# Kernel tuning notes

Measured on AMD Instinct MI355X. Metric: run time of the kernel, lower is better.

The kernel has to match this reference:

```python
import jax, jax.numpy as jnp
import numpy as np

NUM_TABLES = 10  # distinct table_id values per item


def setup_inputs() -> dict:
    key = jax.random.key(0)
    ks = jax.random.split(key, 10)
    B, NL, P, TOK, D = 4, 2, 100, 60, 768
    T = P * TOK
    s = 0.02  # weight init scale
    return {
        "answer_states": jax.random.normal(ks[0], (B, NL, 1, D), jnp.float32),
        "query_passage_states": jax.random.normal(ks[1], (B, NL, T, D), jnp.float32),
        "passage_masks": jax.random.uniform(ks[2], (B, P, TOK), jnp.float32),
        "table_ids": jax.random.randint(ks[3], (B, P), 0, NUM_TABLES, jnp.int32),
        "Wp": jax.random.normal(ks[4], (D, 3 * D), jnp.float32) * s,
        "bp": jnp.zeros((D,), jnp.float32),
        "Wt": jax.random.normal(ks[5], (D, 3 * D), jnp.float32) * s,
        "bt": jnp.zeros((D,), jnp.float32),
        "Wf1": jax.random.normal(ks[6], (D, 2 * D), jnp.float32) * s,
        "bf1": jnp.zeros((D,), jnp.float32),
        "Wf2": jax.random.normal(ks[7], (1, D), jnp.float32) * s,
        "bf2": jnp.zeros((1,), jnp.float32),
    }


def reference(answer_states, query_passage_states, passage_masks, table_ids,
              Wp, bp, Wt, bt, Wf1, bf1, Wf2, bf2):
    # keep only the last layer, as in the torch code ([:, -1:, :, :])
    A = answer_states[:, -1:, :, :]                 # [B,1,1,D]
    Q = query_passage_states[:, -1:, :, :]          # [B,1,T,D]
    A = jnp.broadcast_to(A, Q.shape)                # expand over tokens
    x = jnp.concatenate([A, Q, A * Q], axis=-1)     # [B,1,T,3D]

    ps = jnp.einsum('bltk,dk->bltd', x, Wp) + bp    # passage_fnt  [B,1,T,D]
    ts = jnp.einsum('bltk,dk->bltd', x, Wt) + bt    # table_fnt    [B,1,T,D]

    B, L, T, D = ps.shape
    P, TOK = passage_masks.shape[1], passage_masks.shape[2]
    ps = ps.reshape(B, L, P, TOK, D)
    ts = ts.reshape(B, L, P, TOK, D)

    def table_aggr(states, ids):
        # states: [L,P,TOK,D]; segment-max over passages sharing a table_id,
        # then gather the aggregate back to every passage (the dict grouping).
        s = jnp.moveaxis(states, 1, 0)                       # [P,L,TOK,D]
        tmax = jnp.full((NUM_TABLES,) + s.shape[1:], -jnp.inf, s.dtype)
        tmax = tmax.at[ids].max(s)                           # [NT,L,TOK,D]
        return jnp.moveaxis(tmax[ids], 0, 1)                 # [L,P,TOK,D]

    aggr = jax.vmap(table_aggr)(ts, table_ids)               # [B,L,P,TOK,D]

    feat = jnp.concatenate([ps, aggr], axis=-1)              # [B,L,P,TOK,2D]
    h = jax.nn.relu(jnp.einsum('blptk,dk->blptd', feat, Wf1) + bf1)
    # dropout is identity in eval mode
    scores = (jnp.einsum('blptd,od->blpto', h, Wf2) + bf2)[..., 0]  # [B,L,P,TOK]

    masked = scores * passage_masks[:, None, :, :]           # mask expanded over layers
    return masked.sum(axis=(1, 3))                            # [B,P]
```

## Files before the change

### kernel.cpp

```cpp
#include <hip/hip_runtime.h>
#include <hip/hip_bf16.h>


typedef unsigned short u16;
typedef unsigned int u32;
typedef __attribute__((ext_vector_type(8))) short bf16x8;
typedef __attribute__((ext_vector_type(4))) float f32x4;

#define NUM_TABLES 10
#define MPAD 6016
#define DD 768

__device__ __forceinline__ u16 f2bf(float f) {
  u32 u = __builtin_bit_cast(u32, f);
  u32 r = u + 0x7FFFu + ((u >> 16) & 1u);
  return (u16)(r >> 16);
}
__device__ __forceinline__ float bf2f(u16 h) {
  u32 u = ((u32)h) << 16;
  return __builtin_bit_cast(float, u);
}
__device__ __forceinline__ u32 pack_bf2(float lo, float hi) {
  return (u32)f2bf(lo) | ((u32)f2bf(hi) << 16);
}

__device__ __forceinline__ void gload_lds16(const u16* g, u16* l) {
  __builtin_amdgcn_global_load_lds(
      (const __attribute__((address_space(1))) void*)g,
      (__attribute__((address_space(3))) void*)l, 16, 0, 0);
}

__global__ void prep_all(const float* __restrict__ qps, uint4* __restrict__ qpad,
                         const float* __restrict__ Ans, const float* __restrict__ Wp,
                         const float* __restrict__ Wt, u16* __restrict__ Wtb,
                         u16* __restrict__ WpbT,
                         const float* __restrict__ Wf1, uint4* __restrict__ Wf1b,
                         const float* __restrict__ bp, const float* __restrict__ bt,
                         float* __restrict__ cp, float* __restrict__ ct,
                         const float* __restrict__ mask, const float* __restrict__ bf2,
                         float* __restrict__ out) {
  int blk = blockIdx.x;
  int tid = threadIdx.x;
  if (blk < 9024) {
    size_t c = (size_t)blk * 256 + tid;
    const int per_b = MPAD * (DD / 8);
    int b = (int)(c / per_b);
    int rr = (int)(c % per_b);
    int r = rr / (DD / 8);
    int kc = rr % (DD / 8);
    uint4 o;
    if (r < 6000) {
      const float* src = qps + (((size_t)(b * 2 + 1)) * 6000 + r) * DD + kc * 8;
      float4 f0 = *(const float4*)src;
      float4 f1 = *(const float4*)(src + 4);
      o.x = pack_bf2(f0.x, f0.y);
      o.y = pack_bf2(f0.z, f0.w);
      o.z = pack_bf2(f1.x, f1.y);
      o.w = pack_bf2(f1.z, f1.w);
    } else {
      o = make_uint4(0, 0, 0, 0);
    }
    qpad[c] = o;
  } else if (blk < 10176) {
    size_t c = (size_t)(blk - 9024) * 256 + tid;
    const int per_b = DD * (DD / 8);
    int b = (int)(c / per_b);
    int rr = (int)(c % per_b);
    int d = rr / (DD / 8);
    int k8 = (rr % (DD / 8)) * 8;
    const float* a = Ans + ((size_t)b * 2 + 1) * DD + k8;
    const float* w2r = Wt + (size_t)d * 2304 + 768 + k8;
    const float* w3r = Wt + (size_t)d * 2304 + 1536 + k8;
    float4 a0 = *(const float4*)a, a1 = *(const float4*)(a + 4);
    float4 t20 = *(const float4*)w2r, t21 = *(const float4*)(w2r + 4);
    float4 t30 = *(const float4*)w3r, t31 = *(const float4*)(w3r + 4);
    uint4 o;
    o.x = pack_bf2(t20.x + a0.x * t30.x, t20.y + a0.y * t30.y);
    o.y = pack_bf2(t20.z + a0.z * t30.z, t20.w + a0.w * t30.w);
    o.z = pack_bf2(t21.x + a1.x * t31.x, t21.y + a1.y * t31.y);
    o.w = pack_bf2(t21.z + a1.z * t31.z, t21.w + a1.w * t31.w);
    *(uint4*)(Wtb + ((size_t)b * DD + d) * DD + k8) = o;
  } else if (blk < 10752) {
    int tb = blk - 10176;
    int b = tb / 144;
    int tt = tb % 144;
    int k0 = (tt / 12) * 64, d0 = (tt % 12) * 64;
    __shared__ u16 tile[64][72];
    int kc = tid & 63;
    int r0 = tid >> 6;
    float av = Ans[((size_t)b * 2 + 1) * DD + k0 + kc];
#pragma unroll
    for (int it = 0; it < 16; ++it) {
      int dr = it * 4 + r0;
      const float* wrow = Wp + (size_t)(d0 + dr) * 2304;
      float v = wrow[768 + k0 + kc] + av * wrow[1536 + k0 + kc];
      tile[kc][dr] = f2bf(v);
    }
    __syncthreads();
#pragma unroll
    for (int it = 0; it < 2; ++it) {
      int kk = it * 32 + (tid >> 3);
      int dd = (tid & 7) * 8;
      *(uint4*)(WpbT + ((size_t)b * DD + k0 + kk) * DD + d0 + dd) =
          *(const uint4*)&tile[kk][dd];
    }
  } else if (blk < 11328) {
    size_t c = (size_t)(blk - 10752) * 256 + tid;
    const float* src = Wf1 + c * 8;
    float4 f0 = *(const float4*)src;
    float4 f1 = *(const float4*)(src + 4);
    uint4 o;
    o.x = pack_bf2(f0.x, f0.y);
    o.y = pack_bf2(f0.z, f0.w);
    o.z = pack_bf2(f1.x, f1.y);
    o.w = pack_bf2(f1.z, f1.w);
    Wf1b[c] = o;
  } else if (blk < 12864) {
    int e = blk - 11328;
    int isT = e >= 768;
    int d = e - (isT ? 768 : 0);
    const float* wrow = (isT ? Wt : Wp) + (size_t)d * 2304;
    float a0 = 0.f, a1 = 0.f, a2 = 0.f, a3 = 0.f;
    for (int k = tid; k < DD; k += 256) {
      float w = wrow[k];
      a0 += w * Ans[1 * DD + k];
      a1 += w * Ans[3 * DD + k];
      a2 += w * Ans[5 * DD + k];
      a3 += w * Ans[7 * DD + k];
    }
#pragma unroll
    for (int off = 32; off > 0; off >>= 1) {
      a0 += __shfl_down(a0, off);
      a1 += __shfl_down(a1, off);
      a2 += __shfl_down(a2, off);
      a3 += __shfl_down(a3, off);
    }
    __shared__ float red[4][4];
    int wid = tid >> 6;
    if ((tid & 63) == 0) {
      red[wid][0] = a0; red[wid][1] = a1; red[wid][2] = a2; red[wid][3] = a3;
    }
    __syncthreads();
    if (tid < 4) {
      float s = red[0][tid] + red[1][tid] + red[2][tid] + red[3][tid];
      float bias = (isT ? bt : bp)[d];
      (isT ? ct : cp)[tid * DD + d] = s + bias;
    }
  } else {
    int idx = (blk - 12864) * 256 + tid;
    if (idx >= 400) return;
    const float* m = mask + (size_t)idx * 60;
    float s = 0.f;
    for (int t = 0; t < 60; ++t) s += m[t];
    out[idx] = bf2[0] * s;
  }
}

__global__ __launch_bounds__(256, 2)
void mid_kernel(const u16* __restrict__ Q, const u16* __restrict__ Wtb,
                const float* __restrict__ ct, u16* __restrict__ ts,
                const u16* __restrict__ Wf1b, const u16* __restrict__ WpbT,
                u16* __restrict__ Wcomb, const float* __restrict__ Wf1,
                const float* __restrict__ cp, const float* __restrict__ bf1,
                float* __restrict__ bf1x) {
  __shared__ u16 As[2][128 * 64];
  __shared__ u16 Bs[2][128 * 64];
  __shared__ float red[4][4];
  int blk = blockIdx.x;
  int tid = threadIdx.x;

  if (blk >= 1272) {
    int c = blk - 1272;
    const float* wrow = Wf1 + (size_t)c * 1536;
    float a0 = 0.f, a1 = 0.f, a2 = 0.f, a3 = 0.f;
    for (int d = tid; d < DD; d += 256) {
      float w = wrow[d];
      a0 += w * cp[0 * DD + d];
      a1 += w * cp[1 * DD + d];
      a2 += w * cp[2 * DD + d];
      a3 += w * cp[3 * DD + d];
    }
#pragma unroll
    for (int off = 32; off > 0; off >>= 1) {
      a0 += __shfl_down(a0, off);
      a1 += __shfl_down(a1, off);
      a2 += __shfl_down(a2, off);
      a3 += __shfl_down(a3, off);
    }
    int wid = tid >> 6;
    if ((tid & 63) == 0) {
      red[wid][0] = a0; red[wid][1] = a1; red[wid][2] = a2; red[wid][3] = a3;
    }
    __syncthreads();
    if (tid < 4) {
      float s = red[0][tid] + red[1][tid] + red[2][tid] + red[3][tid];
      bf1x[tid * DD + c] = bf1[c] + s;
    }
    return;
  }

  const int lane = tid & 63;
  const int wid = tid >> 6;
  const int wm = wid >> 1, wn = wid & 1;
  const int lrow = lane >> 3;
  const int lcol_s = (((lane & 7) ^ (lrow & 7)) * 8);
  const int axor = (lane & 7) << 3;
  f32x4 acc[4][4] = {};

  if (blk < 1128) {
    int lid = (blk & 7) * 141 + (blk >> 3);
    int n = lid % 6;
    int m = (lid / 6) % 47;
    int b = lid / 282;
    const int m0 = m * 128;
    const int n0 = n * 128;

    const u16* Abase = Q + (size_t)b * MPAD * DD;
    const u16* Bbase = Wtb + (size_t)b * DD * DD;

    const u16* aptr[4];
    const u16* bptr[4];
#pragma unroll
    for (int j = 0; j < 4; ++j) {
      aptr[j] = Abase + (size_t)(m0 + wid * 32 + j * 8 + lrow) * DD + lcol_s;
      bptr[j] = Bbase + (size_t)(n0 + wid * 32 + j * 8 + lrow) * DD + lcol_s;
    }
#pragma unroll
    for (int j = 0; j < 4; ++j) {
      gload_lds16(aptr[j], &As[0][(wid * 32 + j * 8) * 64]);
      gload_lds16(bptr[j], &Bs[0][(wid * 32 + j * 8) * 64]);
      aptr[j] += 64; bptr[j] += 64;
    }
    __syncthreads();

    int cur = 0;
    for (int kt = 0; kt < 12; ++kt) {
      if (kt < 11) {
#pragma unroll
        for (int j = 0; j < 4; ++j) {
          gload_lds16(aptr[j], &As[cur ^ 1][(wid * 32 + j * 8) * 64]);
          gload_lds16(bptr[j], &Bs[cur ^ 1][(wid * 32 + j * 8) * 64]);
          aptr[j] += 64; bptr[j] += 64;
        }
      }
      bf16x8 af[2][4], bfr[2][4];
#pragma unroll
      for (int kf = 0; kf < 2; ++kf)
#pragma unroll
        for (int mf = 0; mf < 4; ++mf)
          af[kf][mf] = *(const bf16x8*)&As[cur][(wm * 64 + mf * 16 + (lane & 15)) * 64 + ((kf * 32 + (lane >> 4) * 8) ^ axor)];
#pragma unroll
      for (int kf = 0; kf < 2; ++kf)
#pragma unroll
        for (int nf = 0; nf < 4; ++nf)
          bfr[kf][nf] = *(const bf16x8*)&Bs[cur][(wn * 64 + nf * 16 + (lane & 15)) * 64 + ((kf * 32 + (lane >> 4) * 8) ^ axor)];
#pragma unroll
      for (int mf = 0; mf < 4; ++mf)
#pragma unroll
        for (int nf = 0; nf < 4; ++nf) {
          acc[mf][nf] = __builtin_amdgcn_mfma_f32_16x16x32_bf16(af[0][mf], bfr[0][nf], acc[mf][nf], 0, 0, 0);
          acc[mf][nf] = __builtin_amdgcn_mfma_f32_16x16x32_bf16(af[1][mf], bfr[1][nf], acc[mf][nf], 0, 0, 0);
        }
      __syncthreads();
      cur ^= 1;
    }

    u16* dst = ts + (size_t)b * MPAD * DD;
    const float* cv = ct + b * DD;
#pragma unroll
    for (int mf = 0; mf < 4; ++mf)
#pragma unroll
      for (int nf = 0; nf < 4; ++nf)
#pragma unroll
        for (int r = 0; r < 4; ++r) {
          int row = m0 + wm * 64 + mf * 16 + (lane >> 4) * 4 + r;
          int col = n0 + wn * 64 + nf * 16 + (lane & 15);
          dst[(size_t)row * DD + col] = f2bf(acc[mf][nf][r] + cv[col]);
        }
  } else {
    int f = blk - 1128;
    int lid = (f & 7) * 18 + (f >> 3);
    int n = lid % 6;
    int m = (lid / 6) % 6;
    int b = lid / 36;
    const int m0 = m * 128;
    const int n0 = n * 128;

    const u16* Bbase = WpbT + (size_t)b * DD * DD;
    const u16* aptr[4];
    const u16* bptr[4];
#pragma unroll
    for (int j = 0; j < 4; ++j) {
      aptr[j] = Wf1b + (size_t)(m0 + wid * 32 + j * 8 + lrow) * 1536 + lcol_s;
      bptr[j] = Bbase + (size_t)(n0 + wid * 32 + j * 8 + lrow) * DD + lcol_s;
    }
#pragma unroll
    for (int j = 0; j < 4; ++j) {
      gload_lds16(aptr[j], &As[0][(wid * 32 + j * 8) * 64]);
      gload_lds16(bptr[j], &Bs[0][(wid * 32 + j * 8) * 64]);
      aptr[j] += 64; bptr[j] += 64;
    }
    __syncthreads();

    int cur = 0;
    for (int kt = 0; kt < 12; ++kt) {
      if (kt < 11) {
#pragma unroll
        for (int j = 0; j < 4; ++j) {
          gload_lds16(aptr[j], &As[cur ^ 1][(wid * 32 + j * 8) * 64]);
          gload_lds16(bptr[j], &Bs[cur ^ 1][(wid * 32 + j * 8) * 64]);
          aptr[j] += 64; bptr[j] += 64;
        }
      }
      bf16x8 af[2][4], bfr[2][4];
#pragma unroll
      for (int kf = 0; kf < 2; ++kf)
#pragma unroll
        for (int mf = 0; mf < 4; ++mf)
          af[kf][mf] = *(const bf16x8*)&As[cur][(wm * 64 + mf * 16 + (lane & 15)) * 64 + ((kf * 32 + (lane >> 4) * 8) ^ axor)];
#pragma unroll
      for (int kf = 0; kf < 2; ++kf)
#pragma unroll
        for (int nf = 0; nf < 4; ++nf)
          bfr[kf][nf] = *(const bf16x8*)&Bs[cur][(wn * 64 + nf * 16 + (lane & 15)) * 64 + ((kf * 32 + (lane >> 4) * 8) ^ axor)];
#pragma unroll
      for (int mf = 0; mf < 4; ++mf)
#pragma unroll
        for (int nf = 0; nf < 4; ++nf) {
          acc[mf][nf] = __builtin_amdgcn_mfma_f32_16x16x32_bf16(af[0][mf], bfr[0][nf], acc[mf][nf], 0, 0, 0);
          acc[mf][nf] = __builtin_amdgcn_mfma_f32_16x16x32_bf16(af[1][mf], bfr[1][nf], acc[mf][nf], 0, 0, 0);
        }
      __syncthreads();
      cur ^= 1;
    }

    u16* Cb = Wcomb + (size_t)b * DD * DD;
#pragma unroll
    for (int mf = 0; mf < 4; ++mf)
#pragma unroll
      for (int nf = 0; nf < 4; ++nf)
#pragma unroll
        for (int r = 0; r < 4; ++r) {
          int row = m0 + wm * 64 + mf * 16 + (lane >> 4) * 4 + r;
          int col = n0 + wn * 64 + nf * 16 + (lane & 15);
          Cb[(size_t)row * DD + col] = f2bf(acc[mf][nf][r]);
        }
  }
}

__global__ void table_max_kernel(const u16* __restrict__ ts, const int* __restrict__ ids,
                                 u16* __restrict__ tmax) {
  int bi = blockIdx.x;
  int b = bi / 180;
  int rem = bi % 180;
  int tok = rem / 3;
  int dc = rem % 3;
  int d = dc * 256 + threadIdx.x;
  __shared__ int sids[100];
  if (threadIdx.x < 100) sids[threadIdx.x] = ids[b * 100 + threadIdx.x];
  __syncthreads();
  float m[NUM_TABLES];
#pragma unroll
  for (int t = 0; t < NUM_TABLES; ++t) m[t] = -INFINITY;
  const u16* base = ts + ((size_t)b * MPAD + tok) * DD + d;
  for (int p = 0; p < 100; ++p) {
    float v = bf2f(base[(size_t)p * 60 * DD]);
    int id = sids[p];
#pragma unroll
    for (int t = 0; t < NUM_TABLES; ++t)
      if (id == t) m[t] = fmaxf(m[t], v);
  }
#pragma unroll
  for (int t = 0; t < NUM_TABLES; ++t)
    tmax[(((size_t)b * NUM_TABLES + t) * 60 + tok) * DD + d] = f2bf(m[t]);
}

__global__ __launch_bounds__(256, 2)
void gemm_t(const u16* __restrict__ tmax, const u16* __restrict__ Wf1b,
            float* __restrict__ Ht) {
  int flat = blockIdx.x;
  int lid = (flat & 7) * 15 + (flat >> 3);
  int n = lid % 6;
  int m = (lid / 6) % 5;
  int b = lid / 30;

  const int m0 = m * 128;
  const int n0 = n * 128;
  const int tid = threadIdx.x;
  const int lane = tid & 63;
  const int wid = tid >> 6;
  const int wm = wid >> 1, wn = wid & 1;

  __shared__ u16 As[2][128 * 64];
  __shared__ u16 Bs[2][128 * 64];

  const u16* Abase = tmax + (size_t)b * 600 * DD;

  f32x4 acc[4][4] = {};

  const int lrow = lane >> 3;
  const int lcol_s = (((lane & 7) ^ (lrow & 7)) * 8);
  const int axor = (lane & 7) << 3;

  const u16* aptr[4];
  const u16* bptr[4];
#pragma unroll
  for (int j = 0; j < 4; ++j) {
    int row = m0 + wid * 32 + j * 8 + lrow;
    int rp = row < 600 ? row : 599;
    aptr[j] = Abase + (size_t)rp * DD + lcol_s;
    bptr[j] = Wf1b + (size_t)(n0 + wid * 32 + j * 8 + lrow) * 1536 + 768 + lcol_s;
  }

#pragma unroll
  for (int j = 0; j < 4; ++j) {
    gload_lds16(aptr[j], &As[0][(wid * 32 + j * 8) * 64]);
    gload_lds16(bptr[j], &Bs[0][(wid * 32 + j * 8) * 64]);
    aptr[j] += 64; bptr[j] += 64;
  }
  __syncthreads();

  int cur = 0;
  for (int kt = 0; kt < 12; ++kt) {
    if (kt < 11) {
#pragma unroll
      for (int j = 0; j < 4; ++j) {
        gload_lds16(aptr[j], &As[cur ^ 1][(wid * 32 + j * 8) * 64]);
        gload_lds16(bptr[j], &Bs[cur ^ 1][(wid * 32 + j * 8) * 64]);
        aptr[j] += 64; bptr[j] += 64;
      }
    }
    bf16x8 af[2][4], bfr[2][4];
#pragma unroll
    for (int kf = 0; kf < 2; ++kf)
#pragma unroll
      for (int mf = 0; mf < 4; ++mf)
        af[kf][mf] = *(const bf16x8*)&As[cur][(wm * 64 + mf * 16 + (lane & 15)) * 64 + ((kf * 32 + (lane >> 4) * 8) ^ axor)];
#pragma unroll
    for (int kf = 0; kf < 2; ++kf)
#pragma unroll
      for (int nf = 0; nf < 4; ++nf)
        bfr[kf][nf] = *(const bf16x8*)&Bs[cur][(wn * 64 + nf * 16 + (lane & 15)) * 64 + ((kf * 32 + (lane >> 4) * 8) ^ axor)];
#pragma unroll
    for (int mf = 0; mf < 4; ++mf)
#pragma unroll
      for (int nf = 0; nf < 4; ++nf) {
        acc[mf][nf] = __builtin_amdgcn_mfma_f32_16x16x32_bf16(af[0][mf], bfr[0][nf], acc[mf][nf], 0, 0, 0);
        acc[mf][nf] = __builtin_amdgcn_mfma_f32_16x16x32_bf16(af[1][mf], bfr[1][nf], acc[mf][nf], 0, 0, 0);
      }
    __syncthreads();
    cur ^= 1;
  }

  float* Hb = Ht + (size_t)b * 640 * DD;
#pragma unroll
  for (int mf = 0; mf < 4; ++mf)
#pragma unroll
    for (int nf = 0; nf < 4; ++nf)
#pragma unroll
      for (int r = 0; r < 4; ++r) {
        int row = m0 + wm * 64 + mf * 16 + (lane >> 4) * 4 + r;
        int col = n0 + wn * 64 + nf * 16 + (lane & 15);
        Hb[(size_t)row * DD + col] = acc[mf][nf][r];
      }
}

__global__ __launch_bounds__(256, 2)
void gemm_h(const u16* __restrict__ Q, const float* __restrict__ Ht,
            const int* __restrict__ ids, const u16* __restrict__ Wcomb,
            const float* __restrict__ bf1x, const float* __restrict__ w2,
            const float* __restrict__ mask, float* __restrict__ out) {
  int flat = blockIdx.x;
  int lid = (flat & 7) * 141 + (flat >> 3);
  int n = lid % 6;
  int m = (lid / 6) % 47;
  int b = lid / 282;

  const int m0 = m * 128;
  const int n0 = n * 128;
  const int tid = threadIdx.x;
  const int lane = tid & 63;
  const int wid = tid >> 6;
  const int wm = wid >> 1, wn = wid & 1;

  __shared__ u16 As[2][128 * 64];
  __shared__ u16 Bs[2][128 * 64];
  __shared__ int sids[100];
  __shared__ float pacc[4];
  if (tid < 100) sids[tid] = ids[b * 100 + tid];
  if (tid < 4) pacc[tid] = 0.f;
  __syncthreads();

  const u16* Abase = Q + (size_t)b * MPAD * DD;
  const u16* Bbase = Wcomb + (size_t)b * DD * DD;

  f32x4 acc[4][4] = {};

  const int lrow = lane >> 3;
  const int lcol_s = (((lane & 7) ^ (lrow & 7)) * 8);
  const int axor = (lane & 7) << 3;

  const u16* aptr[4];
  const u16* bptr[4];
#pragma unroll
  for (int j = 0; j < 4; ++j) {
    aptr[j] = Abase + (size_t)(m0 + wid * 32 + j * 8 + lrow) * DD + lcol_s;
    bptr[j] = Bbase + (size_t)(n0 + wid * 32 + j * 8 + lrow) * DD + lcol_s;
  }

#pragma unroll
  for (int j = 0; j < 4; ++j) {
    gload_lds16(aptr[j], &As[0][(wid * 32 + j * 8) * 64]);
    gload_lds16(bptr[j], &Bs[0][(wid * 32 + j * 8) * 64]);
    aptr[j] += 64; bptr[j] += 64;
  }
  __syncthreads();

  int cur = 0;
  for (int kt = 0; kt < 12; ++kt) {
    if (kt < 11) {
#pragma unroll
      for (int j = 0; j < 4; ++j) {
        gload_lds16(aptr[j], &As[cur ^ 1][(wid * 32 + j * 8) * 64]);
        gload_lds16(bptr[j], &Bs[cur ^ 1][(wid * 32 + j * 8) * 64]);
        aptr[j] += 64; bptr[j] += 64;
      }
    }
    bf16x8 af[2][4], bfr[2][4];
#pragma unroll
    for (int kf = 0; kf < 2; ++kf)
#pragma unroll
      for (int mf = 0; mf < 4; ++mf)
        af[kf][mf] = *(const bf16x8*)&As[cur][(wm * 64 + mf * 16 + (lane & 15)) * 64 + ((kf * 32 + (lane >> 4) * 8) ^ axor)];
#pragma unroll
    for (int kf = 0; kf < 2; ++kf)
#pragma unroll
      for (int nf = 0; nf < 4; ++nf)
        bfr[kf][nf] = *(const bf16x8*)&Bs[cur][(wn * 64 + nf * 16 + (lane & 15)) * 64 + ((kf * 32 + (lane >> 4) * 8) ^ axor)];
#pragma unroll
    for (int mf = 0; mf < 4; ++mf)
#pragma unroll
      for (int nf = 0; nf < 4; ++nf) {
        acc[mf][nf] = __builtin_amdgcn_mfma_f32_16x16x32_bf16(af[0][mf], bfr[0][nf], acc[mf][nf], 0, 0, 0);
        acc[mf][nf] = __builtin_amdgcn_mfma_f32_16x16x32_bf16(af[1][mf], bfr[1][nf], acc[mf][nf], 0, 0, 0);
      }
    __syncthreads();
    cur ^= 1;
  }

  float b1v[4], w2v[4];
  int cbase = n0 + wn * 64 + (lane & 15);
#pragma unroll
  for (int nf = 0; nf < 4; ++nf) {
    b1v[nf] = bf1x[b * DD + cbase + nf * 16];
    w2v[nf] = w2[cbase + nf * 16];
  }
  const float* Hb = Ht + (size_t)b * 640 * DD;
  const int pfirst = m0 / 60;
#pragma unroll
  for (int mf = 0; mf < 4; ++mf)
#pragma unroll
    for (int r = 0; r < 4; ++r) {
      int row = m0 + wm * 64 + mf * 16 + (lane >> 4) * 4 + r;
      if (row < 6000) {
        int p = (unsigned)row / 60u;
        int tok = row - p * 60;
        const float* htrow = Hb + (size_t)(sids[p] * 60 + tok) * DD + cbase;
        float s = 0.f;
#pragma unroll
        for (int nf = 0; nf < 4; ++nf)
          s += fmaxf(acc[mf][nf][r] + htrow[nf * 16] + b1v[nf], 0.f) * w2v[nf];
        s += __shfl_xor(s, 1);
        s += __shfl_xor(s, 2);
        s += __shfl_xor(s, 4);
        s += __shfl_xor(s, 8);
        if ((lane & 15) == 0) {
          float mk = mask[((size_t)b * 100 + p) * 60 + tok];
          atomicAdd(&pacc[p - pfirst], mk * s);
        }
      }
    }
  __syncthreads();
  int plast = (m0 + 127 < 6000 ? m0 + 127 : 5999) / 60;
  if (tid <= plast - pfirst)
    atomicAdd(out + b * 100 + pfirst + tid, pacc[tid]);
}

extern "C" void kernel_launch(void* const* d_in, const int* in_sizes, int n_in,
                              void* d_out, int out_size, void* d_ws, size_t ws_size,
                              hipStream_t stream) {
  const float* answer = (const float*)d_in[0];
  const float* qps    = (const float*)d_in[1];
  const float* mask   = (const float*)d_in[2];
  const int*   tids   = (const int*)d_in[3];
  const float* Wp     = (const float*)d_in[4];
  const float* bp     = (const float*)d_in[5];
  const float* Wt     = (const float*)d_in[6];
  const float* bt     = (const float*)d_in[7];
  const float* Wf1    = (const float*)d_in[8];
  const float* bf1    = (const float*)d_in[9];
  const float* Wf2    = (const float*)d_in[10];
  const float* bf2    = (const float*)d_in[11];
  float* out = (float*)d_out;

  char* ws = (char*)d_ws;
  u16* Qpad  = (u16*)(ws + 0);
  u16* ts    = (u16*)(ws + 36962304);
  u16* tmax  = (u16*)(ws + 73924608);
  float* Ht  = (float*)(ws + 77611008);
  u16* Wtb   = (u16*)(ws + 85475328);
  u16* WpbT  = (u16*)(ws + 90193920);
  u16* Wcomb = (u16*)(ws + 94912512);
  u16* Wf1b  = (u16*)(ws + 99631104);
  float* cp  = (float*)(ws + 101990400);
  float* ct  = (float*)(ws + 102002688);
  float* bf1x= (float*)(ws + 102014976);

  prep_all<<<12866, 256, 0, stream>>>(qps, (uint4*)Qpad, answer, Wp, Wt, Wtb, WpbT,
                                      Wf1, (uint4*)Wf1b, bp, bt, cp, ct,
                                      mask, bf2, out);

  mid_kernel<<<2040, 256, 0, stream>>>(Qpad, Wtb, ct, ts, Wf1b, WpbT, Wcomb,
                                       Wf1, cp, bf1, bf1x);

  table_max_kernel<<<720, 256, 0, stream>>>(ts, tids, tmax);

  gemm_t<<<120, 256, 0, stream>>>(tmax, Wf1b, Ht);

  gemm_h<<<1128, 256, 0, stream>>>(Qpad, Ht, tids, Wcomb, bf1x, Wf2, mask, out);
}
```

Baseline: 200.4 us.

## Merge table GEMM into main GEMM with ticket-based inter-block dependency

Fuses the small gemm_t kernel (120 tiles) into gemm_h. The first 120 blocks to grab an atomic ticket compute Ht tiles, publish them with a fence and increment a completion counter. Every block then runs its Q×Wcomb GEMM and spin-waits on that counter before the epilogue reads Ht. This removes one kernel launch and the idle tail of the small GEMM, letting the table GEMM overlap the main one. It adds a spin-wait and a cross-block dependency that relies on forward progress of the ticket-holding blocks. Both counters are reset to zero in prep_all.

```diff
diff --git a/kernel.cpp b/kernel.cpp
--- a/kernel.cpp
+++ b/kernel.cpp
@@ -38,7 +38,7 @@
                          const float* __restrict__ bp, const float* __restrict__ bt,
                          float* __restrict__ cp, float* __restrict__ ct,
                          const float* __restrict__ mask, const float* __restrict__ bf2,
-                         float* __restrict__ out) {
+                         float* __restrict__ out, u32* __restrict__ sync) {
   int blk = blockIdx.x;
   int tid = threadIdx.x;
   if (blk < 9024) {
@@ -148,7 +148,10 @@
     }
   } else {
     int idx = (blk - 12864) * 256 + tid;
-    if (idx >= 400) return;
+    if (idx >= 400) {
+      if (idx < 402) sync[idx - 400] = 0u;
+      return;
+    }
     const float* m = mask + (size_t)idx * 60;
     float s = 0.f;
     for (int t = 0; t < 60; ++t) s += m[t];
@@ -376,214 +379,210 @@
 }
 
 __global__ __launch_bounds__(256, 2)
-void gemm_t(const u16* __restrict__ tmax, const u16* __restrict__ Wf1b,
-            float* __restrict__ Ht) {
-  int flat = blockIdx.x;
-  int lid = (flat & 7) * 15 + (flat >> 3);
-  int n = lid % 6;
-  int m = (lid / 6) % 5;
-  int b = lid / 30;
-
-  const int m0 = m * 128;
-  const int n0 = n * 128;
+void gemm_ht(const u16* __restrict__ Q, const u16* __restrict__ tmax,
+             const u16* __restrict__ Wf1b, float* __restrict__ Ht,
+             const int* __restrict__ ids, const u16* __restrict__ Wcomb,
+             const float* __restrict__ bf1x, const float* __restrict__ w2,
+             const float* __restrict__ mask, float* __restrict__ out,
+             u32* __restrict__ sync) {
+  __shared__ u16 As[2][128 * 64];
+  __shared__ u16 Bs[2][128 * 64];
+  __shared__ int sids[100];
+  __shared__ float pacc[4];
+  __shared__ u32 tkt;
   const int tid = threadIdx.x;
   const int lane = tid & 63;
   const int wid = tid >> 6;
   const int wm = wid >> 1, wn = wid & 1;
-
-  __shared__ u16 As[2][128 * 64];
-  __shared__ u16 Bs[2][128 * 64];
-
-  const u16* Abase = tmax + (size_t)b * 600 * DD;
-
-  f32x4 acc[4][4] = {};
-
   const int lrow = lane >> 3;
   const int lcol_s = (((lane & 7) ^ (lrow & 7)) * 8);
   const int axor = (lane & 7) << 3;
 
-  const u16* aptr[4];
-  const u16* bptr[4];
-#pragma unroll
-  for (int j = 0; j < 4; ++j) {
-    int row = m0 + wid * 32 + j * 8 + lrow;
-    int rp = row < 600 ? row : 599;
-    aptr[j] = Abase + (size_t)rp * DD + lcol_s;
-    bptr[j] = Wf1b + (size_t)(n0 + wid * 32 + j * 8 + lrow) * 1536 + 768 + lcol_s;
+  if (tid == 0) tkt = atomicAdd(&sync[0], 1u);
+  __syncthreads();
+  const u32 myt = tkt;
+
+  if (myt < 120) {
+    int lid = (myt & 7) * 15 + (myt >> 3);
+    int n = lid % 6;
+    int m = (lid / 6) % 5;
+    int b = lid / 30;
+    const int m0 = m * 128;
+    const int n0 = n * 128;
+
+    const u16* Abase = tmax + (size_t)b * 600 * DD;
+    f32x4 acc[4][4] = {};
+    const u16* aptr[4];
+    const u16* bptr[4];
+#pragma unroll
+    for (int j = 0; j < 4; ++j) {
+      int row = m0 + wid * 32 + j * 8 + lrow;
+      int rp = row < 600 ? row : 599;
+      aptr[j] = Abase + (size_t)rp * DD + lcol_s;
+      bptr[j] = Wf1b + (size_t)(n0 + wid * 32 + j * 8 + lrow) * 1536 + 768 + lcol_s;
+    }
+#pragma unroll
+    for (int j = 0; j < 4; ++j) {
+      gload_lds16(aptr[j], &As[0][(wid * 32 + j * 8) * 64]);
+      gload_lds16(bptr[j], &Bs[0][(wid * 32 + j * 8) * 64]);
+      aptr[j] += 64; bptr[j] += 64;
+    }
+    __syncthreads();
+
+    int cur = 0;
+    for (int kt = 0; kt < 12; ++kt) {
+      if (kt < 11) {
+#pragma unroll
+        for (int j = 0; j < 4; ++j) {
+          gload_lds16(aptr[j], &As[cur ^ 1][(wid * 32 + j * 8) * 64]);
+          gload_lds16(bptr[j], &Bs[cur ^ 1][(wid * 32 + j * 8) * 64]);
+          aptr[j] += 64; bptr[j] += 64;
+        }
+      }
+      bf16x8 af[2][4], bfr[2][4];
+#pragma unroll
+      for (int kf = 0; kf < 2; ++kf)
+#pragma unroll
+        for (int mf = 0; mf < 4; ++mf)
+          af[kf][mf] = *(const bf16x8*)&As[cur][(wm * 64 + mf * 16 + (lane & 15)) * 64 + ((kf * 32 + (lane >> 4) * 8) ^ axor)];
+#pragma unroll
+      for (int kf = 0; kf < 2; ++kf)
+#pragma unroll
+        for (int nf = 0; nf < 4; ++nf)
+          bfr[kf][nf] = *(const bf16x8*)&Bs[cur][(wn * 64 + nf * 16 + (lane & 15)) * 64 + ((kf * 32 + (lane >> 4) * 8) ^ axor)];
+#pragma unroll
+      for (int mf = 0; mf < 4; ++mf)
+#pragma unroll
+        for (int nf = 0; nf < 4; ++nf) {
+          acc[mf][nf] = __builtin_amdgcn_mfma_f32_16x16x32_bf16(af[0][mf], bfr[0][nf], acc[mf][nf], 0, 0, 0);
+          acc[mf][nf] = __builtin_amdgcn_mfma_f32_16x16x32_bf16(af[1][mf], bfr[1][nf], acc[mf][nf], 0, 0, 0);
+        }
+      __syncthreads();
+      cur ^= 1;
+    }
+
+    float* Hb = Ht + (size_t)b * 640 * DD;
+#pragma unroll
+    for (int mf = 0; mf < 4; ++mf)
+#pragma unroll
+      for (int nf = 0; nf < 4; ++nf)
+#pragma unroll
+        for (int r = 0; r < 4; ++r) {
+          int row = m0 + wm * 64 + mf * 16 + (lane >> 4) * 4 + r;
+          int col = n0 + wn * 64 + nf * 16 + (lane & 15);
+          Hb[(size_t)row * DD + col] = acc[mf][nf][r];
+        }
+    __threadfence();
+    __syncthreads();
+    if (tid == 0) atomicAdd(&sync[1], 1u);
   }
 
-#pragma unroll
-  for (int j = 0; j < 4; ++j) {
-    gload_lds16(aptr[j], &As[0][(wid * 32 + j * 8) * 64]);
-    gload_lds16(bptr[j], &Bs[0][(wid * 32 + j * 8) * 64]);
-    aptr[j] += 64; bptr[j] += 64;
-  }
-  __syncthreads();
-
-  int cur = 0;
-  for (int kt = 0; kt < 12; ++kt) {
-    if (kt < 11) {
-#pragma unroll
-      for (int j = 0; j < 4; ++j) {
-        gload_lds16(aptr[j], &As[cur ^ 1][(wid * 32 + j * 8) * 64]);
-        gload_lds16(bptr[j], &Bs[cur ^ 1][(wid * 32 + j * 8) * 64]);
-        aptr[j] += 64; bptr[j] += 64;
+  {
+    int blk = blockIdx.x;
+    int lid = (blk & 7) * 141 + (blk >> 3);
+    int n = lid % 6;
+    int m = (lid / 6) % 47;
+    int b = lid / 282;
+    const int m0 = m * 128;
+    const int n0 = n * 128;
+
+    if (tid < 100) sids[tid] = ids[b * 100 + tid];
+    if (tid < 4) pacc[tid] = 0.f;
+
+    const u16* Abase = Q + (size_t)b * MPAD * DD;
+    const u16* Bbase = Wcomb + (size_t)b * DD * DD;
+
+    f32x4 acc[4][4] = {};
+    const u16* aptr[4];
+    const u16* bptr[4];
+#pragma unroll
+    for (int j = 0; j < 4; ++j) {
+      aptr[j] = Abase + (size_t)(m0 + wid * 32 + j * 8 + lrow) * DD + lcol_s;
+      bptr[j] = Bbase + (size_t)(n0 + wid * 32 + j * 8 + lrow) * DD + lcol_s;
+    }
+#pragma unroll
+    for (int j = 0; j < 4; ++j) {
+      gload_lds16(aptr[j], &As[0][(wid * 32 + j * 8) * 64]);
+      gload_lds16(bptr[j], &Bs[0][(wid * 32 + j * 8) * 64]);
+      aptr[j] += 64; bptr[j] += 64;
+    }
+    __syncthreads();
+
+    int cur = 0;
+    for (int kt = 0; kt < 12; ++kt) {
+      if (kt < 11) {
+#pragma unroll
+        for (int j = 0; j < 4; ++j) {
+          gload_lds16(aptr[j], &As[cur ^ 1][(wid * 32 + j * 8) * 64]);
+          gload_lds16(bptr[j], &Bs[cur ^ 1][(wid * 32 + j * 8) * 64]);
+          aptr[j] += 64; bptr[j] += 64;
+        }
       }
-    }
-    bf16x8 af[2][4], bfr[2][4];
-#pragma unroll
-    for (int kf = 0; kf < 2; ++kf)
+      bf16x8 af[2][4], bfr[2][4];
+#pragma unroll
+      for (int kf = 0; kf < 2; ++kf)
+#pragma unroll
+        for (int mf = 0; mf < 4; ++mf)
+          af[kf][mf] = *(const bf16x8*)&As[cur][(wm * 64 + mf * 16 + (lane & 15)) * 64 + ((kf * 32 + (lane >> 4) * 8) ^ axor)];
+#pragma unroll
+      for (int kf = 0; kf < 2; ++kf)
+#pragma unroll
+        for (int nf = 0; nf < 4; ++nf)
+          bfr[kf][nf] = *(const bf16x8*)&Bs[cur][(wn * 64 + nf * 16 + (lane & 15)) * 64 + ((kf * 32 + (lane >> 4) * 8) ^ axor)];
 #pragma unroll
       for (int mf = 0; mf < 4; ++mf)
-        af[kf][mf] = *(const bf16x8*)&As[cur][(wm * 64 + mf * 16 + (lane & 15)) * 64 + ((kf * 32 + (lane >> 4) * 8) ^ axor)];
-#pragma unroll
-    for (int kf = 0; kf < 2; ++kf)
-#pragma unroll
-      for (int nf = 0; nf < 4; ++nf)
-        bfr[kf][nf] = *(const bf16x8*)&Bs[cur][(wn * 64 + nf * 16 + (lane & 15)) * 64 + ((kf * 32 + (lane >> 4) * 8) ^ axor)];
+#pragma unroll
+        for (int nf = 0; nf < 4; ++nf) {
+          acc[mf][nf] = __builtin_amdgcn_mfma_f32_16x16x32_bf16(af[0][mf], bfr[0][nf], acc[mf][nf], 0, 0, 0);
+          acc[mf][nf] = __builtin_amdgcn_mfma_f32_16x16x32_bf16(af[1][mf], bfr[1][nf], acc[mf][nf], 0, 0, 0);
+        }
+      __syncthreads();
+      cur ^= 1;
+    }
+
+    if (tid == 0) {
+      while (atomicAdd(&sync[1], 0u) < 120u) __builtin_amdgcn_s_sleep(32);
+    }
+    __syncthreads();
+    __threadfence();
+
+    float b1v[4], w2v[4];
+    int cbase = n0 + wn * 64 + (lane & 15);
+#pragma unroll
+    for (int nf = 0; nf < 4; ++nf) {
+      b1v[nf] = bf1x[b * DD + cbase + nf * 16];
+      w2v[nf] = w2[cbase + nf * 16];
+    }
+    const float* Hb = Ht + (size_t)b * 640 * DD;
+    const int pfirst = m0 / 60;
 #pragma unroll
     for (int mf = 0; mf < 4; ++mf)
-#pragma unroll
-      for (int nf = 0; nf < 4; ++nf) {
-        acc[mf][nf] = __builtin_amdgcn_mfma_f32_16x16x32_bf16(af[0][mf], bfr[0][nf], acc[mf][nf], 0, 0, 0);
-        acc[mf][nf] = __builtin_amdgcn_mfma_f32_16x16x32_bf16(af[1][mf], bfr[1][nf], acc[mf][nf], 0, 0, 0);
-      }
-    __syncthreads();
-    cur ^= 1;
-  }
-
-  float* Hb = Ht + (size_t)b * 640 * DD;
-#pragma unroll
-  for (int mf = 0; mf < 4; ++mf)
-#pragma unroll
-    for (int nf = 0; nf < 4; ++nf)
 #pragma unroll
       for (int r = 0; r < 4; ++r) {
         int row = m0 + wm * 64 + mf * 16 + (lane >> 4) * 4 + r;
-        int col = n0 + wn * 64 + nf * 16 + (lane & 15);
-        Hb[(size_t)row * DD + col] = acc[mf][nf][r];
+        if (row < 6000) {
+          int p = (unsigned)row / 60u;
+          int tok = row - p * 60;
+          const float* htrow = Hb + (size_t)(sids[p] * 60 + tok) * DD + cbase;
+          float s = 0.f;
+#pragma unroll
+          for (int nf = 0; nf < 4; ++nf)
+            s += fmaxf(acc[mf][nf][r] + htrow[nf * 16] + b1v[nf], 0.f) * w2v[nf];
+          s += __shfl_xor(s, 1);
+          s += __shfl_xor(s, 2);
+          s += __shfl_xor(s, 4);
+          s += __shfl_xor(s, 8);
+          if ((lane & 15) == 0) {
+            float mk = mask[((size_t)b * 100 + p) * 60 + tok];
+            atomicAdd(&pacc[p - pfirst], mk * s);
+          }
+        }
       }
-}
-
-__global__ __launch_bounds__(256, 2)
-void gemm_h(const u16* __restrict__ Q, const float* __restrict__ Ht,
-            const int* __restrict__ ids, const u16* __restrict__ Wcomb,
-            const float* __restrict__ bf1x, const float* __restrict__ w2,
-            const float* __restrict__ mask, float* __restrict__ out) {
-  int flat = blockIdx.x;
-  int lid = (flat & 7) * 141 + (flat >> 3);
-  int n = lid % 6;
-  int m = (lid / 6) % 47;
-  int b = lid / 282;
-
-  const int m0 = m * 128;
-  const int n0 = n * 128;
-  const int tid = threadIdx.x;
-  const int lane = tid & 63;
-  const int wid = tid >> 6;
-  const int wm = wid >> 1, wn = wid & 1;
-
-  __shared__ u16 As[2][128 * 64];
-  __shared__ u16 Bs[2][128 * 64];
-  __shared__ int sids[100];
-  __shared__ float pacc[4];
-  if (tid < 100) sids[tid] = ids[b * 100 + tid];
-  if (tid < 4) pacc[tid] = 0.f;
-  __syncthreads();
-
-  const u16* Abase = Q + (size_t)b * MPAD * DD;
-  const u16* Bbase = Wcomb + (size_t)b * DD * DD;
-
-  f32x4 acc[4][4] = {};
-
-  const int lrow = lane >> 3;
-  const int lcol_s = (((lane & 7) ^ (lrow & 7)) * 8);
-  const int axor = (lane & 7) << 3;
-
-  const u16* aptr[4];
-  const u16* bptr[4];
-#pragma unroll
-  for (int j = 0; j < 4; ++j) {
-    aptr[j] = Abase + (size_t)(m0 + wid * 32 + j * 8 + lrow) * DD + lcol_s;
-    bptr[j] = Bbase + (size_t)(n0 + wid * 32 + j * 8 + lrow) * DD + lcol_s;
+    __syncthreads();
+    int plast = (m0 + 127 < 6000 ? m0 + 127 : 5999) / 60;
+    if (tid <= plast - pfirst)
+      atomicAdd(out + b * 100 + pfirst + tid, pacc[tid]);
   }
-
-#pragma unroll
-  for (int j = 0; j < 4; ++j) {
-    gload_lds16(aptr[j], &As[0][(wid * 32 + j * 8) * 64]);
-    gload_lds16(bptr[j], &Bs[0][(wid * 32 + j * 8) * 64]);
-    aptr[j] += 64; bptr[j] += 64;
-  }
-  __syncthreads();
-
-  int cur = 0;
-  for (int kt = 0; kt < 12; ++kt) {
-    if (kt < 11) {
-#pragma unroll
-      for (int j = 0; j < 4; ++j) {
-        gload_lds16(aptr[j], &As[cur ^ 1][(wid * 32 + j * 8) * 64]);
-        gload_lds16(bptr[j], &Bs[cur ^ 1][(wid * 32 + j * 8) * 64]);
-        aptr[j] += 64; bptr[j] += 64;
-      }
-    }
-    bf16x8 af[2][4], bfr[2][4];
-#pragma unroll
-    for (int kf = 0; kf < 2; ++kf)
-#pragma unroll
-      for (int mf = 0; mf < 4; ++mf)
-        af[kf][mf] = *(const bf16x8*)&As[cur][(wm * 64 + mf * 16 + (lane & 15)) * 64 + ((kf * 32 + (lane >> 4) * 8) ^ axor)];
-#pragma unroll
-    for (int kf = 0; kf < 2; ++kf)
-#pragma unroll
-      for (int nf = 0; nf < 4; ++nf)
-        bfr[kf][nf] = *(const bf16x8*)&Bs[cur][(wn * 64 + nf * 16 + (lane & 15)) * 64 + ((kf * 32 + (lane >> 4) * 8) ^ axor)];
-#pragma unroll
-    for (int mf = 0; mf < 4; ++mf)
-#pragma unroll
-      for (int nf = 0; nf < 4; ++nf) {
-        acc[mf][nf] = __builtin_amdgcn_mfma_f32_16x16x32_bf16(af[0][mf], bfr[0][nf], acc[mf][nf], 0, 0, 0);
-        acc[mf][nf] = __builtin_amdgcn_mfma_f32_16x16x32_bf16(af[1][mf], bfr[1][nf], acc[mf][nf], 0, 0, 0);
-      }
-    __syncthreads();
-    cur ^= 1;
-  }
-
-  float b1v[4], w2v[4];
-  int cbase = n0 + wn * 64 + (lane & 15);
-#pragma unroll
-  for (int nf = 0; nf < 4; ++nf) {
-    b1v[nf] = bf1x[b * DD + cbase + nf * 16];
-    w2v[nf] = w2[cbase + nf * 16];
-  }
-  const float* Hb = Ht + (size_t)b * 640 * DD;
-  const int pfirst = m0 / 60;
-#pragma unroll
-  for (int mf = 0; mf < 4; ++mf)
-#pragma unroll
-    for (int r = 0; r < 4; ++r) {
-      int row = m0 + wm * 64 + mf * 16 + (lane >> 4) * 4 + r;
-      if (row < 6000) {
-        int p = (unsigned)row / 60u;
-        int tok = row - p * 60;
-        const float* htrow = Hb + (size_t)(sids[p] * 60 + tok) * DD + cbase;
-        float s = 0.f;
-#pragma unroll
-        for (int nf = 0; nf < 4; ++nf)
-          s += fmaxf(acc[mf][nf][r] + htrow[nf * 16] + b1v[nf], 0.f) * w2v[nf];
-        s += __shfl_xor(s, 1);
-        s += __shfl_xor(s, 2);
-        s += __shfl_xor(s, 4);
-        s += __shfl_xor(s, 8);
-        if ((lane & 15) == 0) {
-          float mk = mask[((size_t)b * 100 + p) * 60 + tok];
-          atomicAdd(&pacc[p - pfirst], mk * s);
-        }
-      }
-    }
-  __syncthreads();
-  int plast = (m0 + 127 < 6000 ? m0 + 127 : 5999) / 60;
-  if (tid <= plast - pfirst)
-    atomicAdd(out + b * 100 + pfirst + tid, pacc[tid]);
 }
 
 extern "C" void kernel_launch(void* const* d_in, const int* in_sizes, int n_in,
@@ -615,17 +614,17 @@
   float* cp  = (float*)(ws + 101990400);
   float* ct  = (float*)(ws + 102002688);
   float* bf1x= (float*)(ws + 102014976);
+  u32* sync  = (u32*)(ws + 102027264);
 
   prep_all<<<12866, 256, 0, stream>>>(qps, (uint4*)Qpad, answer, Wp, Wt, Wtb, WpbT,
                                       Wf1, (uint4*)Wf1b, bp, bt, cp, ct,
-                                      mask, bf2, out);
+                                      mask, bf2, out, sync);
 
   mid_kernel<<<2040, 256, 0, stream>>>(Qpad, Wtb, ct, ts, Wf1b, WpbT, Wcomb,
                                        Wf1, cp, bf1, bf1x);
 
   table_max_kernel<<<720, 256, 0, stream>>>(ts, tids, tmax);
 
-  gemm_t<<<120, 256, 0, stream>>>(tmax, Wf1b, Ht);
-
-  gemm_h<<<1128, 256, 0, stream>>>(Qpad, Ht, tids, Wcomb, bf1x, Wf2, mask, out);
-}
+  gemm_ht<<<1128, 256, 0, stream>>>(Qpad, tmax, Wf1b, Ht, tids, Wcomb,
+                                    bf1x, Wf2, mask, out, sync);
+}
```

New measurement: 313.6 us. +56.4%, slower.
